# Kernel tuning notes

Measured on AMD Instinct MI355X. Metric: run time of the kernel, lower is better.

## Reference

```python
import jax, jax.numpy as jnp
import numpy as np

N, E, Z, C, B, G, T = 10000, 160000, 10, 64, 8, 16, 2
R_MAX = 5.0
AVG_NEIGH = 16.0
L_SLICES = ((0, 1), (1, 4), (4, 9))  # l=0,1,2 blocks of the 9 SH components


def sph_harm(u):
    # component-normalized real spherical harmonics up to l=2, u: [E,3] unit vectors
    x, y, z = u[:, 0], u[:, 1], u[:, 2]
    s3, s5, s15 = 3.0 ** 0.5, 5.0 ** 0.5, 15.0 ** 0.5
    return jnp.stack([
        jnp.ones_like(x),
        s3 * x, s3 * y, s3 * z,
        s15 * x * y, s15 * y * z, (s5 / 2) * (3 * z * z - 1), s15 * x * z, (s15 / 2) * (x * x - y * y),
    ], axis=1)  # [E,9]


def radial_embed(r):
    # Bessel basis * polynomial cutoff (p=5), r: [E]
    u = r / R_MAX
    n = jnp.arange(1, B + 1, dtype=jnp.float32)
    bessel = jnp.sqrt(2.0 / R_MAX) * jnp.sin(n[None, :] * jnp.pi * u[:, None]) / (r[:, None] + 1e-9)
    p = 5.0
    fc = 1 - (p + 1) * (p + 2) / 2 * u ** p + p * (p + 2) * u ** (p + 1) - p * (p + 1) / 2 * u ** (p + 2)
    fc = jnp.where(u < 1.0, fc, 0.0)
    return bessel * fc[:, None]  # [E,B]


def per_l_linear(x, W):
    # x: [n,C,9], W: [3,C,C]; independent channel mixing per l-block
    return jnp.concatenate([
        jnp.einsum('ncm,cd->ndm', x[:, :, s:e], W[l]) for l, (s, e) in enumerate(L_SLICES)
    ], axis=2)


def _forward(positions, node_attrs, charges, shifts, W_emb, atomic_energies,
             W_r1, W_r2, W_mix, W_sc, w_poly, W_prod, w_e, w_d,
             edge_index, batch, num_graphs):
    sender, receiver = edge_index[0], edge_index[1]
    # atomic reference energies
    node_e0 = node_attrs @ atomic_energies  # [N]
    e0 = jax.ops.segment_sum(node_e0, batch, num_segments=num_graphs)
    # node embedding: scalars only
    node_feats = jnp.zeros((positions.shape[0], C, 9), positions.dtype)
    node_feats = node_feats.at[:, :, 0].set(node_attrs @ W_emb)
    # edge geometry
    vec = positions[sender] - positions[receiver] + shifts  # [E,3]
    lengths = jnp.sqrt(jnp.sum(vec * vec, axis=1) + 1e-12)
    sh = sph_harm(vec / lengths[:, None])        # [E,9]
    edge_feats = radial_embed(lengths)           # [E,B]
    energies = [e0]
    dipoles = []
    for t in range(T):
        # radial MLP -> per-channel TP weights
        w = jax.nn.silu(edge_feats @ W_r1[t]) @ W_r2[t]      # [E,C]
        h_s = node_feats[sender, :, 0]                       # gather sender scalars [E,C]
        m = (w * h_s)[:, :, None] * sh[:, None, :]           # TP message [E,C,9]
        agg = jax.ops.segment_sum(m, receiver, num_segments=positions.shape[0]) / AVG_NEIGH
        msg = per_l_linear(agg, W_mix[t])
        sc = per_l_linear(node_feats, W_sc[t])               # self-connection
        # product basis (correlation 3): channel-wise scalar polynomial gate
        s0 = msg[:, :, 0]
        poly = w_poly[t, :, 0][None] + w_poly[t, :, 1][None] * s0 + w_poly[t, :, 2][None] * s0 * s0
        node_feats = per_l_linear(msg * poly[:, :, None], W_prod[t]) + sc
        # readout: 1x0e energy + 1x1o dipole
        e_n = node_feats[:, :, 0] @ w_e[t]                   # [N]
        energies.append(jax.ops.segment_sum(e_n, batch, num_segments=num_graphs))
        dipoles.append(jnp.einsum('ncm,c->nm', node_feats[:, :, 1:4], w_d[t]))  # [N,3]
    contributions = jnp.stack(energies, axis=-1)             # [G,T+1]
    total_energy = jnp.sum(contributions, axis=-1)           # [G]
    atomic_dipoles = jnp.sum(jnp.stack(dipoles, axis=-1), axis=-1)  # [N,3]
    total_dipole = jax.ops.segment_sum(atomic_dipoles, batch, num_segments=num_graphs)
    total_dipole = total_dipole + jax.ops.segment_sum(charges[:, None] * positions, batch, num_segments=num_graphs)
    return total_energy, contributions, atomic_dipoles, total_dipole


def setup_inputs():
    key = jax.random.key(0)
    ks = jax.random.split(key, 16)
    s = 0.1
    species = jax.random.randint(ks[1], (N,), 0, Z)
    return {
        'positions': jax.random.normal(ks[0], (N, 3)) * 3.0,
        'node_attrs': jax.nn.one_hot(species, Z, dtype=jnp.float32),
        'charges': jax.random.normal(ks[2], (N,)) * 0.1,
        'shifts': jnp.zeros((E, 3), jnp.float32),
        'W_emb': jax.random.normal(ks[5], (Z, C)) * s,
        'atomic_energies': jax.random.normal(ks[6], (Z,)) * s,
        'W_r1': jax.random.normal(ks[7], (T, B, 64)) * s,
        'W_r2': jax.random.normal(ks[8], (T, 64, C)) * s,
        'W_mix': jax.random.normal(ks[9], (T, 3, C, C)) * s,
        'W_sc': jax.random.normal(ks[10], (T, 3, C, C)) * s,
        'w_poly': jax.random.normal(ks[11], (T, C, 3)) * s,
        'W_prod': jax.random.normal(ks[12], (T, 3, C, C)) * s,
        'w_e': jax.random.normal(ks[13], (T, C)) * s,
        'w_d': jax.random.normal(ks[14], (T, C)) * s,
        'edge_index': jax.random.randint(ks[3], (2, E), 0, N),
        'batch': jnp.sort(jax.random.randint(ks[4], (N,), 0, G)),
        'num_graphs': G,
    }


def reference(positions, node_attrs, charges, shifts, W_emb, atomic_energies,
              W_r1, W_r2, W_mix, W_sc, w_poly, W_prod, w_e, w_d,
              edge_index, batch, num_graphs):
    args = (node_attrs, charges, shifts, W_emb, atomic_energies, W_r1, W_r2,
            W_mix, W_sc, w_poly, W_prod, w_e, w_d, edge_index, batch, num_graphs)
    total_energy, contributions, atomic_dipoles, total_dipole = _forward(positions, *args)
    forces = -jax.grad(lambda p: jnp.sum(_forward(p, *args)[0]))(positions)
    return total_energy, contributions, forces, total_dipole, atomic_dipoles
```

## Files before the change

kernel.cpp:

```cpp
#include <hip/hip_runtime.h>
#include <hip/hip_bf16.h>

#define NN 10000
#define NE 160000
#define NZ 10
#define NBES 8
#define NG 16
#define NT 2
#define NB 2048
#define NB1 2049
#define PL ((size_t)NN*64)

static constexpr float PI_F  = 3.14159265358979323846f;
static constexpr float KBES  = 0.63245553203367587f;
static constexpr float S3    = 1.73205080756887729f;

static constexpr size_t OFF_UVL  = 0;
static constexpr size_t OFF_PIN  = OFF_UVL + (size_t)NE*4;
static constexpr size_t OFF_ATT  = OFF_PIN + (size_t)NN*3;
static constexpr size_t OFF_CHG  = OFF_ATT + (size_t)NN*NZ;
static constexpr size_t OFF_SHF  = OFF_CHG + (size_t)NN;
static constexpr size_t OFF_NF0  = OFF_SHF + (size_t)NE*3;
static constexpr size_t OFF_NF1  = OFF_NF0 + PL;
static constexpr size_t OFF_MSG0 = OFF_NF1 + 4*PL;
static constexpr size_t OFF_MSG1 = OFF_MSG0 + PL;
static constexpr size_t OFF_AGG  = OFF_MSG1 + PL;
static constexpr size_t O_GA1    = OFF_AGG;
static constexpr size_t O_GA0    = OFF_AGG + 2*PL;
static constexpr size_t OFF_W    = OFF_AGG + 4*PL;
static constexpr size_t O_WEMB   = OFF_W;
static constexpr size_t O_AE     = O_WEMB + 640;
static constexpr size_t O_R1     = O_AE   + 16;
static constexpr size_t O_R2     = O_R1   + 1024;
static constexpr size_t O_WMIX   = O_R2   + 8192;
static constexpr size_t O_WMIXT  = O_WMIX + 24576;
static constexpr size_t O_WSC    = O_WMIXT+ 24576;
static constexpr size_t O_WSCT   = O_WSC  + 24576;
static constexpr size_t O_WPROD  = O_WSCT + 24576;
static constexpr size_t O_WPRODT = O_WPROD+ 24576;
static constexpr size_t O_WPOLY  = O_WPRODT+24576;
static constexpr size_t O_WE     = O_WPOLY+ 384;
static constexpr size_t O_WD     = O_WE   + 128;
static constexpr size_t OFF_ACC  = O_WD   + 128;
static constexpr size_t O_E0G    = OFF_ACC;
static constexpr size_t O_ETG    = O_E0G + 16;
static constexpr size_t O_TD     = O_ETG + 32;
static constexpr size_t O_ADP    = O_TD  + 48;
static constexpr size_t O_GPOS   = O_ADP + (size_t)NN*3;
static constexpr size_t ACC_FLOATS = 96 + (size_t)NN*6;
static constexpr size_t O_EN0    = O_GPOS + (size_t)NN*3;
static constexpr size_t O_EN1    = O_EN0 + NN;
static constexpr size_t O_E0N    = O_EN1 + NN;
static constexpr size_t O_FLAG   = O_E0N + NN;
static constexpr size_t O_TW     = O_FLAG + 4;
static constexpr size_t O_TQ     = O_TW + (size_t)2*NB1*64;
static constexpr size_t O_OFFR   = O_TQ + (size_t)2*NB1*64;
static constexpr size_t O_OFFS   = O_OFFR + (NN+1);
static constexpr size_t O_CURR   = O_OFFS + (NN+1);
static constexpr size_t O_CURS   = O_CURR + NN;
static constexpr size_t O_RECRAW = O_CURS + NN;
static constexpr size_t O_RECR   = (O_RECRAW + 7) & ~(size_t)7;
static constexpr size_t O_RECS   = O_RECR + (size_t)NE*8;
static constexpr size_t WS_FLOATS= O_RECS + (size_t)NE*8;

__device__ __forceinline__ float rlane(float v, int l){
  return __int_as_float(__builtin_amdgcn_readlane(__float_as_int(v), l));
}

static constexpr int LD_CNT[14] = {NN*3, NN*NZ, NN, NE*3, NZ*64, NZ, NT*NBES*64, NT*64*64,
                                   NT*3*64*64, NT*3*64*64, NT*64*3, NT*3*64*64, NT*64, NT*64};
static constexpr int LD_TOTAL = NN*3 + NN*NZ + NN + NE*3 + NZ*64 + NZ + NT*NBES*64 + NT*64*64
                              + 3*(NT*3*64*64) + NT*64*3 + 4*(NT*64) - NT*64*2;
__global__ __launch_bounds__(256) void k_load_all(
    const void* s0, const void* s1, const void* s2, const void* s3, const void* s4,
    const void* s5, const void* s6, const void* s7, const void* s8, const void* s9,
    const void* s10, const void* s11, const void* s12, const void* s13,
    float* __restrict__ ws){
  __shared__ int found;
  if (threadIdx.x == 0) found = 0;
  __syncthreads();
  const unsigned* raw = (const unsigned*)s1;
  int f = 0;
  for (int i = threadIdx.x; i < 4096; i += 256){
    unsigned w = raw[i];
    f |= (w == 0x00003F80u || w == 0x3F803F80u) ? 1 : 0;
  }
  if (f) found = 1;
  __syncthreads();
  const int isbf = found;
  if (blockIdx.x == 0 && threadIdx.x == 0) ((int*)(ws + O_FLAG))[0] = isbf;

  const void* srcs[14] = {s0,s1,s2,s3,s4,s5,s6,s7,s8,s9,s10,s11,s12,s13};
  const size_t dsts[14] = {OFF_PIN, OFF_ATT, OFF_CHG, OFF_SHF, O_WEMB, O_AE, O_R1, O_R2,
                           O_WMIX, O_WSC, O_WPOLY, O_WPROD, O_WE, O_WD};
  int i = blockIdx.x*256 + threadIdx.x;
  int seg = -1, off = i;
  #pragma unroll
  for (int j = 0; j < 14; ++j){
    if (seg < 0){
      if (off < LD_CNT[j]) seg = j;
      else off -= LD_CNT[j];
    }
  }
  if (seg < 0) return;
  float v = isbf ? __bfloat162float(((const __hip_bfloat16*)srcs[seg])[off])
                 : ((const float*)srcs[seg])[off];
  ws[dsts[seg] + off] = v;
}

static constexpr int GEOM_B = (NE+255)/256;
static constexpr int TAB_B  = (2*NB1+3)/4;
static constexpr int INIT_B = (NN+3)/4;
static constexpr int TRAN_B = 5*4096/256;
__global__ __launch_bounds__(256, 3) void k_prep(float* __restrict__ ws, const int* __restrict__ ei){
  int b = blockIdx.x;
  if (b < GEOM_B){
    int e = b*256 + threadIdx.x;
    if (e >= NE) return;
    const float* pos = ws + OFF_PIN;
    const float* shifts = ws + OFF_SHF;
    int s = ei[e], r = ei[NE + e];
    float vx = pos[s*3+0] - pos[r*3+0] + shifts[(size_t)e*3+0];
    float vy = pos[s*3+1] - pos[r*3+1] + shifts[(size_t)e*3+1];
    float vz = pos[s*3+2] - pos[r*3+2] + shifts[(size_t)e*3+2];
    float L = sqrtf(vx*vx + vy*vy + vz*vz + 1e-12f);
    float inv = 1.f / L;
    float4 uq; uq.x = vx*inv; uq.y = vy*inv; uq.z = vz*inv; uq.w = L;
    *(float4*)(ws + OFF_UVL + (size_t)e*4) = uq;
    if (L < 5.f){
      atomicAdd((int*)(ws + O_CURR) + r, 1);
      atomicAdd((int*)(ws + O_CURS) + s, 1);
    }
  } else if (b < GEOM_B + TAB_B){
    int lane = threadIdx.x & 63;
    int task = (b - GEOM_B)*4 + (threadIdx.x >> 6);
    if (task >= 2*NB1) return;
    int t = task / NB1, node = task % NB1;
    const float* R1 = ws + O_R1 + (size_t)t*512;
    const float* R2 = ws + O_R2 + (size_t)t*4096;
    float r1c[8];
    #pragma unroll
    for (int j = 0; j < 8; ++j) r1c[j] = R1[j*64 + lane];
    float L = fmaxf((float)node * (5.f/NB), 1e-6f);
    float ur = L*0.2f;
    float ef[8], dd[8];
    if (ur < 1.f){
      float u2=ur*ur, u4=u2*u2, u5=u4*ur;
      float fc = 1.f - 21.f*u5 + 35.f*u5*ur - 15.f*u5*u2;
      float omu = 1.f - ur;
      float dfc = -105.f*u4*omu*omu;
      float invr = 1.f/(L + 1e-9f);
      #pragma unroll
      for (int bb = 0; bb < 8; ++bb){
        float nb = (float)(bb+1);
        float arg = nb*PI_F*ur;
        float sn = __sinf(arg), cs = __cosf(arg);
        float bes = KBES*sn*invr;
        float dbes = KBES*(nb*PI_F*0.2f)*cs*invr - bes*invr;
        ef[bb] = bes*fc;
        dd[bb] = dbes*fc + bes*dfc*0.2f;
      }
    } else {
      #pragma unroll
      for (int bb = 0; bb < 8; ++bb){ ef[bb] = 0.f; dd[bb] = 0.f; }
    }
    float a = 0.f, tt = 0.f;
    #pragma unroll
    for (int bb = 0; bb < 8; ++bb){ a = fmaf(ef[bb], r1c[bb], a); tt = fmaf(r1c[bb], dd[bb], tt); }
    float sg = 1.f/(1.f + __expf(-a));
    float sl = a*sg;
    float q  = sg*fmaf(a, 1.f - sg, 1.f)*tt;
    float r2c[64];
    #pragma unroll
    for (int j = 0; j < 64; ++j) r2c[j] = R2[j*64 + lane];
    float W0=0.f, W1=0.f, Q0=0.f, Q1=0.f;
    #pragma unroll
    for (int j = 0; j < 64; j += 2){
      W0 = fmaf(rlane(sl, j  ), r2c[j  ], W0);
      W1 = fmaf(rlane(sl, j+1), r2c[j+1], W1);
      Q0 = fmaf(rlane(q,  j  ), r2c[j  ], Q0);
      Q1 = fmaf(rlane(q,  j+1), r2c[j+1], Q1);
    }
    size_t idx = ((size_t)t*NB1 + node)*64 + lane;
    ws[O_TW + idx] = (W0+W1)*(1.f/16.f);
    ws[O_TQ + idx] = (Q0+Q1)*(1.f/16.f);
  } else if (b < GEOM_B + TAB_B + INIT_B){
    int lane = threadIdx.x & 63;
    int n = (b - GEOM_B - TAB_B)*4 + (threadIdx.x >> 6);
    if (n >= NN) return;
    const float* attrs = ws + OFF_ATT;
    float acc = 0.f;
    #pragma unroll
    for (int z = 0; z < NZ; ++z) acc = fmaf(attrs[(size_t)n*NZ+z], ws[O_WEMB + z*64 + lane], acc);
    ws[OFF_NF0 + (size_t)n*64 + lane] = acc;
    if (lane == 0){
      float e = 0.f;
      #pragma unroll
      for (int z = 0; z < NZ; ++z) e = fmaf(attrs[(size_t)n*NZ+z], ws[O_AE + z], e);
      ws[O_E0N + n] = e;
    }
  } else {
    int i = (b - GEOM_B - TAB_B - INIT_B)*256 + threadIdx.x;
    int mat = i >> 12, r = (i >> 6) & 63, c = i & 63;
    const size_t src[5] = {O_WMIX, O_WMIX+12288, O_WPROD, O_WPROD+12288, O_WSC+12288};
    const size_t dst[5] = {O_WMIXT, O_WMIXT+12288, O_WPRODT, O_WPRODT+12288, O_WSCT+12288};
    ws[dst[mat] + (size_t)c*64 + r] = ws[src[mat] + (size_t)r*64 + c];
  }
}

__global__ __launch_bounds__(1024) void k_csr_scan(
    int* __restrict__ curr, int* __restrict__ curs,
    int* __restrict__ offr, int* __restrict__ offs_){
  __shared__ unsigned short cr[NN], cs[NN];
  __shared__ int pr[1024], ps[1024];
  int tid = threadIdx.x;
  for (int i = tid; i < NN; i += 1024){
    cr[i] = (unsigned short)curr[i];
    cs[i] = (unsigned short)curs[i];
  }
  __syncthreads();
  const int chunk = (NN + 1023)/1024;
  int lo = tid*chunk, hi = lo + chunk;
  if (hi > NN) hi = NN;
  if (lo > NN) lo = NN;
  int sr = 0, ss = 0;
  for (int i = lo; i < hi; ++i){ sr += cr[i]; ss += cs[i]; }
  pr[tid] = sr; ps[tid] = ss;
  __syncthreads();
  for (int o = 1; o < 1024; o <<= 1){
    int vr = (tid >= o) ? pr[tid-o] : 0;
    int vs = (tid >= o) ? ps[tid-o] : 0;
    __syncthreads();
    pr[tid] += vr; ps[tid] += vs;
    __syncthreads();
  }
  int runr = tid ? pr[tid-1] : 0;
  int runs = tid ? ps[tid-1] : 0;
  for (int i = lo; i < hi; ++i){
    int a = cr[i], c = cs[i];
    offr[i] = runr; curr[i] = runr; runr += a;
    offs_[i] = runs; curs[i] = runs; runs += c;
  }
  if (tid == 1023){ offr[NN] = runr; offs_[NN] = runs; }
}

__global__ void k_csr_fill(const int* __restrict__ ei, const float* __restrict__ uvl,
                           int* __restrict__ curr, int* __restrict__ curs,
                           float* __restrict__ recr, float* __restrict__ recs){
  int e = blockIdx.x*256 + threadIdx.x;
  if (e >= NE) return;
  float4 q = *(const float4*)(uvl + (size_t)e*4);
  if (q.w >= 5.f) return;
  int s = ei[e], r = ei[NE + e];
  int4 meta; meta.x = s; meta.y = r; meta.z = e; meta.w = 0;
  int pr = atomicAdd(&curr[r], 1);
  *(float4*)(recr + (size_t)pr*8) = q;
  *(int4*)(recr + (size_t)pr*8 + 4) = meta;
  int ps = atomicAdd(&curs[s], 1);
  *(float4*)(recs + (size_t)ps*8) = q;
  *(int4*)(recs + (size_t)ps*8 + 4) = meta;
}

__global__ __launch_bounds__(256) void k_agg(
    const float* __restrict__ TWt, const float* __restrict__ recr,
    const float* __restrict__ h, const int* __restrict__ offr,
    float* __restrict__ agg){
  int lane = threadIdx.x & 63;
  int wid = blockIdx.x*4 + (threadIdx.x >> 6);
  int nw  = gridDim.x*4;
  for (int n = wid; n < NN; n += nw){
    int lo = offr[n], hi = offr[n+1];
    float c0=0.f, x1=0.f, y1=0.f, z1=0.f;
    float d0=0.f, x2=0.f, y2=0.f, z2=0.f;
    int i = lo;
    for (; i+1 < hi; i += 2){
      const float4 qa = *(const float4*)(recr + (size_t)i*8);
      const int sa = __builtin_amdgcn_readfirstlane(((const int*)(recr + (size_t)i*8 + 4))[0]);
      const float4 qb = *(const float4*)(recr + (size_t)(i+1)*8);
      const int sb = __builtin_amdgcn_readfirstlane(((const int*)(recr + (size_t)(i+1)*8 + 4))[0]);
      float pa = qa.w*(NB/5.f); int ba = (int)pa; float fa = pa - (float)ba;
      float pb = qb.w*(NB/5.f); int bbq = (int)pb; float fb = pb - (float)bbq;
      const float* Ta = TWt + (size_t)ba*64 + lane;
      const float* Tb = TWt + (size_t)bbq*64 + lane;
      float ta0 = Ta[0], tb0 = Tb[0];
      float wa = fmaf(Ta[64]-ta0, fa, ta0);
      float wb = fmaf(Tb[64]-tb0, fb, tb0);
      float wha = wa * h[(size_t)sa*64 + lane];
      float whb = wb * h[(size_t)sb*64 + lane];
      c0 += wha; d0 += whb;
      x1 = fmaf(wha, qa.x, x1); x2 = fmaf(whb, qb.x, x2);
      y1 = fmaf(wha, qa.y, y1); y2 = fmaf(whb, qb.y, y2);
      z1 = fmaf(wha, qa.z, z1); z2 = fmaf(whb, qb.z, z2);
    }
    if (i < hi){
      const float4 q = *(const float4*)(recr + (size_t)i*8);
      const int sU = __builtin_amdgcn_readfirstlane(((const int*)(recr + (size_t)i*8 + 4))[0]);
      float pa = q.w*(NB/5.f); int ba = (int)pa; float fa = pa - (float)ba;
      const float* Ta = TWt + (size_t)ba*64 + lane;
      float ta0 = Ta[0];
      float wa = fmaf(Ta[64]-ta0, fa, ta0);
      float wha = wa * h[(size_t)sU*64 + lane];
      c0 += wha;
      x1 = fmaf(wha, q.x, x1);
      y1 = fmaf(wha, q.y, y1);
      z1 = fmaf(wha, q.z, z1);
    }
    size_t ob = (size_t)n*64 + lane;
    agg[ob]        = c0 + d0;
    agg[ob+PL]     = S3*(x1 + x2);
    agg[ob+2*PL]   = S3*(y1 + y2);
    agg[ob+3*PL]   = S3*(z1 + z2);
  }
}

static constexpr int NODE_GRID = 512;
template<int TI>
__global__ __launch_bounds__(256, 2) void k_node(float* __restrict__ ws){
  __shared__ float s0buf[2][64];
  const int lane = threadIdx.x & 63;
  const int k = threadIdx.x >> 6;
  const int l = (k==0) ? 0 : 1;
  const float* Wm = ws + O_WMIX  + TI*12288 + (size_t)l*4096;
  const float* Wp = ws + O_WPROD + TI*12288 + (size_t)l*4096;
  const float* Wsc= ws + O_WSC   + TI*12288 + (size_t)l*4096;
  const bool use_sc = (TI==1) || (k==0);
  float wcm[64], wcp[64], wcs[64];
  #pragma unroll
  for (int j = 0; j < 64; ++j) wcm[j] = Wm[j*64 + lane];
  #pragma unroll
  for (int j = 0; j < 64; ++j) wcp[j] = Wp[j*64 + lane];
  if (use_sc){
    #pragma unroll
    for (int j = 0; j < 64; ++j) wcs[j] = Wsc[j*64 + lane];
  }
  const float p0 = ws[O_WPOLY + TI*192 + lane*3];
  const float p1 = ws[O_WPOLY + TI*192 + lane*3 + 1];
  const float p2 = ws[O_WPOLY + TI*192 + lane*3 + 2];
  const float rw = (k==0) ? ws[O_WE + TI*64 + lane] : ws[O_WD + TI*64 + lane];
  const float* aggk = ws + OFF_AGG + (size_t)k*PL;
  const float* nfk  = (TI==0) ? (ws + OFF_NF0) : (ws + OFF_NF1 + (size_t)k*PL);
  float* msgp = ws + (TI==0 ? OFF_MSG0 : OFF_MSG1);
  float* nfo  = ws + OFF_NF1 + (size_t)k*PL;
  float* en   = ws + (TI==0 ? O_EN0 : O_EN1);
  float* adp  = ws + O_ADP;
  int it = 0;
  for (int n = blockIdx.x; n < NN; n += NODE_GRID, ++it){
    size_t base = (size_t)n*64 + lane;
    float a = aggk[base];
    float m0=0.f, m1=0.f, m2=0.f, m3=0.f;
    #pragma unroll
    for (int j = 0; j < 64; j += 4){
      m0 = fmaf(rlane(a, j  ), wcm[j  ], m0);
      m1 = fmaf(rlane(a, j+1), wcm[j+1], m1);
      m2 = fmaf(rlane(a, j+2), wcm[j+2], m2);
      m3 = fmaf(rlane(a, j+3), wcm[j+3], m3);
    }
    float m = (m0+m1) + (m2+m3);
    if (k == 0) s0buf[it & 1][lane] = m;
    __syncthreads();
    float s0 = s0buf[it & 1][lane];
    float xg = m * fmaf(fmaf(p2, s0, p1), s0, p0);
    float b0=0.f, b1=0.f;
    #pragma unroll
    for (int j = 0; j < 64; j += 2){
      b0 = fmaf(rlane(xg, j  ), wcp[j  ], b0);
      b1 = fmaf(rlane(xg, j+1), wcp[j+1], b1);
    }
    float out = b0 + b1;
    if (use_sc){
      float xs = nfk[base];
      float a0=0.f, a1=0.f;
      #pragma unroll
      for (int j = 0; j < 64; j += 2){
        a0 = fmaf(rlane(xs, j  ), wcs[j  ], a0);
        a1 = fmaf(rlane(xs, j+1), wcs[j+1], a1);
      }
      out += a0 + a1;
    }
    if (TI == 0) nfo[base] = out;
    if (k == 0) msgp[base] = s0;
    float red = out * rw;
    #pragma unroll
    for (int o = 32; o; o >>= 1) red += __shfl_xor(red, o, 64);
    if (lane == 0){
      if (k == 0) en[n] = red;
      else        adp[n*3 + (k-1)] += red;
    }
  }
}

__global__ __launch_bounds__(256, 3) void k_gback1(
    const float* __restrict__ WPRODT1, const float* __restrict__ we1,
    const float* __restrict__ msg1, const float* __restrict__ wp,
    const float* __restrict__ WMIXT1, float* __restrict__ out){
  int lane = threadIdx.x & 63;
  float wcol[64];
  #pragma unroll
  for (int j = 0; j < 64; ++j) wcol[j] = WMIXT1[j*64 + lane];
  float g = 0.f;
  #pragma unroll
  for (int c = 0; c < 64; ++c) g = fmaf(we1[c], WPRODT1[c*64 + lane], g);
  float p0 = wp[lane*3], p1 = wp[lane*3+1], p2 = wp[lane*3+2];
  int wid = blockIdx.x*4 + (threadIdx.x >> 6);
  int nw  = gridDim.x*4;
  for (int n = wid; n < NN; n += nw){
    float s0 = msg1[(size_t)n*64 + lane];
    float poly = fmaf(fmaf(p2, s0, p1), s0, p0);
    float dp   = fmaf(2.f*p2, s0, p1);
    float gb = g*fmaf(s0, dp, poly);
    float a0=0.f, a1=0.f, a2=0.f, a3=0.f;
    #pragma unroll
    for (int j = 0; j < 64; j += 4){
      a0 = fmaf(rlane(gb, j  ), wcol[j  ], a0);
      a1 = fmaf(rlane(gb, j+1), wcol[j+1], a1);
      a2 = fmaf(rlane(gb, j+2), wcol[j+2], a2);
      a3 = fmaf(rlane(gb, j+3), wcol[j+3], a3);
    }
    out[(size_t)n*64 + lane] = (a0+a1) + (a2+a3);
  }
}

static constexpr int GHG_GRID = 1024;
static constexpr int RED_B = (NN+255)/256;
__global__ __launch_bounds__(256) void k_ghg0(float* __restrict__ ws, const int* __restrict__ offs_,
                                              const int* __restrict__ batch){
  __shared__ float wl[2*4096];
  if (blockIdx.x >= GHG_GRID){
    int n = (blockIdx.x - GHG_GRID)*256 + threadIdx.x;
    int lane = threadIdx.x & 63;
    bool valid = (n < NN);
    int g = valid ? batch[n] : -1;
    float v0=0.f, v1=0.f, v2=0.f, tx=0.f, ty=0.f, tz=0.f;
    if (valid){
      v0 = ws[O_E0N + n]; v1 = ws[O_EN0 + n]; v2 = ws[O_EN1 + n];
      float qq = ws[OFF_CHG + n];
      tx = ws[O_ADP + n*3+0] + qq*ws[OFF_PIN + n*3+0];
      ty = ws[O_ADP + n*3+1] + qq*ws[OFF_PIN + n*3+1];
      tz = ws[O_ADP + n*3+2] + qq*ws[OFF_PIN + n*3+2];
    }
    float* e0g = ws + O_E0G; float* Etg = ws + O_ETG; float* td = ws + O_TD;
    int g0 = __shfl(g, 0, 64), g63 = __shfl(g, 63, 64);
    if (g0 == g63 && g0 >= 0){
      #pragma unroll
      for (int o = 32; o; o >>= 1){
        v0 += __shfl_xor(v0, o, 64); v1 += __shfl_xor(v1, o, 64); v2 += __shfl_xor(v2, o, 64);
        tx += __shfl_xor(tx, o, 64); ty += __shfl_xor(ty, o, 64); tz += __shfl_xor(tz, o, 64);
      }
      if (lane == 0){
        atomicAdd(&e0g[g0], v0); atomicAdd(&Etg[g0], v1); atomicAdd(&Etg[16+g0], v2);
        atomicAdd(&td[g0*3+0], tx); atomicAdd(&td[g0*3+1], ty); atomicAdd(&td[g0*3+2], tz);
      }
    } else if (valid){
      atomicAdd(&e0g[g], v0); atomicAdd(&Etg[g], v1); atomicAdd(&Etg[16+g], v2);
      atomicAdd(&td[g*3+0], tx); atomicAdd(&td[g*3+1], ty); atomicAdd(&td[g*3+2], tz);
    }
    return;
  }
  for (int i = threadIdx.x; i < 4096; i += 256){
    wl[i]        = ws[O_WPRODT + i];
    wl[4096 + i] = ws[O_WMIXT + i];
  }
  __syncthreads();
  const int lane = threadIdx.x & 63;
  int wid = blockIdx.x*4 + (threadIdx.x >> 6);
  const int nw = GHG_GRID*4;
  float gnfc = ws[O_WE + lane];
  {
    const float* WS1 = ws + O_WSCT + 12288;
    const float* we1 = ws + O_WE + 64;
    #pragma unroll
    for (int c = 0; c < 64; ++c) gnfc = fmaf(we1[c], WS1[c*64 + lane], gnfc);
  }
  const float p0 = ws[O_WPOLY + lane*3];
  const float p1 = ws[O_WPOLY + lane*3 + 1];
  const float p2 = ws[O_WPOLY + lane*3 + 2];
  const float* TW1 = ws + O_TW + (size_t)NB1*64;
  const float* recs = ws + O_RECS;
  const float* GA1 = ws + O_GA1;
  for (int n = wid; n < NN; n += nw){
    int lo = offs_[n], hi = offs_[n+1];
    float acc = 0.f, acc2 = 0.f;
    int i = lo;
    for (; i+1 < hi; i += 2){
      const float4 qa = *(const float4*)(recs + (size_t)i*8);
      const int ra = __builtin_amdgcn_readfirstlane(((const int*)(recs + (size_t)i*8 + 4))[1]);
      const float4 qb = *(const float4*)(recs + (size_t)(i+1)*8);
      const int rb = __builtin_amdgcn_readfirstlane(((const int*)(recs + (size_t)(i+1)*8 + 4))[1]);
      float pa = qa.w*(NB/5.f); int ba = (int)pa; float fa = pa - (float)ba;
      float pb = qb.w*(NB/5.f); int bbq = (int)pb; float fb = pb - (float)bbq;
      const float* Ta = TW1 + (size_t)ba*64 + lane;
      const float* Tb = TW1 + (size_t)bbq*64 + lane;
      float ta0 = Ta[0], tb0 = Tb[0];
      float wa = fmaf(Ta[64]-ta0, fa, ta0);
      float wb = fmaf(Tb[64]-tb0, fb, tb0);
      acc  = fmaf(wa, GA1[(size_t)ra*64 + lane], acc);
      acc2 = fmaf(wb, GA1[(size_t)rb*64 + lane], acc2);
    }
    if (i < hi){
      const float4 q = *(const float4*)(recs + (size_t)i*8);
      const int rU = __builtin_amdgcn_readfirstlane(((const int*)(recs + (size_t)i*8 + 4))[1]);
      float pa = q.w*(NB/5.f); int ba = (int)pa; float fa = pa - (float)ba;
      const float* Ta = TW1 + (size_t)ba*64 + lane;
      float ta0 = Ta[0];
      float wa = fmaf(Ta[64]-ta0, fa, ta0);
      acc = fmaf(wa, GA1[(size_t)rU*64 + lane], acc);
    }
    float gB = gnfc + (acc + acc2);
    float q0=0.f, q1=0.f;
    #pragma unroll
    for (int j = 0; j < 64; j += 2){
      q0 = fmaf(rlane(gB,j),   wl[j*64 + lane],     q0);
      q1 = fmaf(rlane(gB,j+1), wl[(j+1)*64 + lane], q1);
    }
    float gmp = q0 + q1;
    float s0v = ws[OFF_MSG0 + (size_t)n*64 + lane];
    float poly = fmaf(fmaf(p2, s0v, p1), s0v, p0);
    float dp   = fmaf(2.f*p2, s0v, p1);
    float gb = gmp * fmaf(s0v, dp, poly);
    float u0=0.f, u1=0.f;
    #pragma unroll
    for (int j = 0; j < 64; j += 2){
      u0 = fmaf(rlane(gb,j),   wl[4096 + j*64 + lane],     u0);
      u1 = fmaf(rlane(gb,j+1), wl[4096 + (j+1)*64 + lane], u1);
    }
    ws[O_GA0 + (size_t)n*64 + lane] = u0 + u1;
  }
}

__global__ __launch_bounds__(256) void k_bwdE2(float* __restrict__ ws, const int* __restrict__ nlive_ptr){
  const int lane = threadIdx.x & 63;
  int wid = blockIdx.x*4 + (threadIdx.x >> 6);
  const int nw = gridDim.x*4;
  const int nlive = nlive_ptr[0];
  const float* recs = ws + O_RECS;
  const float* TQ  = ws + O_TQ;
  const float* h0  = ws + OFF_NF0;
  const float* h1  = ws + OFF_NF1;
  const float* ga0 = ws + O_GA0;
  const float* ga1 = ws + O_GA1;
  float* gpos = ws + O_GPOS;
  for (int i = wid; i < nlive; i += nw){
    const float4 q = *(const float4*)(recs + (size_t)i*8);
    const int* meta = (const int*)(recs + (size_t)i*8 + 4);
    const int s = __builtin_amdgcn_readfirstlane(meta[0]);
    const int r = __builtin_amdgcn_readfirstlane(meta[1]);
    float posb = q.w*(NB/5.f);
    int bi = (int)posb;
    float fr = posb - (float)bi;
    const float* T0 = TQ + (size_t)bi*64 + lane;
    const float* T1 = T0 + (size_t)NB1*64;
    float Q0 = fmaf(T0[64]-T0[0], fr, T0[0]);
    float Q1 = fmaf(T1[64]-T1[0], fr, T1[0]);
    float rr = Q0*h0[(size_t)s*64 + lane]*ga0[(size_t)r*64 + lane]
             + Q1*h1[(size_t)s*64 + lane]*ga1[(size_t)r*64 + lane];
    #pragma unroll
    for (int o = 32; o; o >>= 1) rr += __shfl_xor(rr, o, 64);
    if (lane < 3){
      float u = (lane==0) ? q.x : ((lane==1) ? q.y : q.z);
      float v = rr*u;
      atomicAdd(&gpos[(size_t)s*3 + lane],  v);
      atomicAdd(&gpos[(size_t)r*3 + lane], -v);
    }
  }
}

__global__ void k_writeout(const float* __restrict__ e0g, const float* __restrict__ Etg,
                           const float* __restrict__ td, const float* __restrict__ adp,
                           const float* __restrict__ gpos, void* __restrict__ outv,
                           const int* __restrict__ flag){
  int i = blockIdx.x*256 + threadIdx.x;
  const int total = NG + NG*3 + NN*3 + NG*3 + NN*3;
  if (i >= total) return;
  float v;
  if (i < 16){
    v = e0g[i] + Etg[i] + Etg[16+i];
  } else if (i < 64){
    int j = i - 16; int g = j/3, t = j - g*3;
    v = (t == 0) ? e0g[g] : Etg[(t-1)*16 + g];
  } else if (i < 64 + NN*3){
    v = -gpos[i-64];
  } else if (i < 64 + NN*3 + 48){
    v = td[i - (64 + NN*3)];
  } else {
    v = adp[i - (64 + NN*3 + 48)];
  }
  if (flag[0]) ((__hip_bfloat16*)outv)[i] = __float2bfloat16(v);
  else         ((float*)outv)[i] = v;
}

extern "C" void kernel_launch(void* const* d_in, const int* in_sizes, int n_in,
                              void* d_out, int out_size, void* d_ws, size_t ws_size,
                              hipStream_t stream) {
  if (ws_size < WS_FLOATS*sizeof(float)) return;
  const int* ei    = (const int*)d_in[14];
  const int* batch = (const int*)d_in[15];
  float* ws = (float*)d_ws;

  int* offr  = (int*)(ws + O_OFFR);
  int* offs_ = (int*)(ws + O_OFFS);
  int* curr  = (int*)(ws + O_CURR);
  int* curs  = (int*)(ws + O_CURS);

  hipMemsetAsync(ws + OFF_ACC, 0, ACC_FLOATS*sizeof(float), stream);
  hipMemsetAsync(curr, 0, 2*NN*sizeof(int), stream);

  k_load_all<<<(LD_TOTAL+255)/256, 256, 0, stream>>>(
      d_in[0], d_in[1], d_in[2], d_in[3], d_in[4], d_in[5], d_in[6], d_in[7],
      d_in[8], d_in[9], d_in[10], d_in[11], d_in[12], d_in[13], ws);
  k_prep<<<GEOM_B + TAB_B + INIT_B + TRAN_B, 256, 0, stream>>>(ws, ei);
  k_csr_scan<<<1, 1024, 0, stream>>>(curr, curs, offr, offs_);
  k_csr_fill<<<(NE+255)/256, 256, 0, stream>>>(ei, ws+OFF_UVL, curr, curs,
                                               ws+O_RECR, ws+O_RECS);

  k_agg<<<1024, 256, 0, stream>>>(ws+O_TW, ws+O_RECR, ws+OFF_NF0, offr, ws+OFF_AGG);
  k_node<0><<<NODE_GRID, 256, 0, stream>>>(ws);
  k_agg<<<1024, 256, 0, stream>>>(ws+O_TW + (size_t)NB1*64, ws+O_RECR, ws+OFF_NF1, offr, ws+OFF_AGG);
  k_node<1><<<NODE_GRID, 256, 0, stream>>>(ws);

  k_gback1<<<1024, 256, 0, stream>>>(ws+O_WPRODT+12288, ws+O_WE+64,
                                     ws+OFF_MSG1, ws+O_WPOLY+192,
                                     ws+O_WMIXT+12288, ws+O_GA1);
  k_ghg0<<<GHG_GRID + RED_B, 256, 0, stream>>>(ws, offs_, batch);
  k_bwdE2<<<2048, 256, 0, stream>>>(ws, offs_ + NN);

  k_writeout<<<(60112+255)/256, 256, 0, stream>>>(ws+O_E0G, ws+O_ETG, ws+O_TD, ws+O_ADP,
                                                  ws+O_GPOS, d_out, (const int*)(ws+O_FLAG));
}
```

Baseline: 345.6 us.

## Split node channel-mixing across two waves per l-block and prefetch next node

The node-update kernel now uses 512 threads per block, with two waves sharing each of the four l-blocks. Each wave holds half of the weight columns (32 instead of 64 per matrix), and partial sums are combined through shared memory. The next node's aggregate and self-connection inputs are also prefetched into registers before the current node is computed. The aim is to cut per-thread register pressure and per-node latency so more waves hide memory latency, at the cost of a second __syncthreads per node and extra shared-memory traffic.

```diff
diff --git a/kernel.cpp b/kernel.cpp
--- a/kernel.cpp
+++ b/kernel.cpp
@@ -315,23 +315,27 @@
 
 static constexpr int NODE_GRID = 512;
 template<int TI>
-__global__ __launch_bounds__(256, 2) void k_node(float* __restrict__ ws){
-  __shared__ float s0buf[2][64];
+__global__ __launch_bounds__(512, 1) void k_node(float* __restrict__ ws){
+  __shared__ float pm[4][2][64];
+  __shared__ float po[4][2][64];
   const int lane = threadIdx.x & 63;
-  const int k = threadIdx.x >> 6;
+  const int w = threadIdx.x >> 6;
+  const int k = w >> 1;
+  const int h = w & 1;
   const int l = (k==0) ? 0 : 1;
+  const int j0 = h*32;
   const float* Wm = ws + O_WMIX  + TI*12288 + (size_t)l*4096;
   const float* Wp = ws + O_WPROD + TI*12288 + (size_t)l*4096;
   const float* Wsc= ws + O_WSC   + TI*12288 + (size_t)l*4096;
   const bool use_sc = (TI==1) || (k==0);
-  float wcm[64], wcp[64], wcs[64];
+  float wcm[32], wcp[32], wcs[32];
   #pragma unroll
-  for (int j = 0; j < 64; ++j) wcm[j] = Wm[j*64 + lane];
+  for (int j = 0; j < 32; ++j) wcm[j] = Wm[(j0+j)*64 + lane];
   #pragma unroll
-  for (int j = 0; j < 64; ++j) wcp[j] = Wp[j*64 + lane];
+  for (int j = 0; j < 32; ++j) wcp[j] = Wp[(j0+j)*64 + lane];
   if (use_sc){
     #pragma unroll
-    for (int j = 0; j < 64; ++j) wcs[j] = Wsc[j*64 + lane];
+    for (int j = 0; j < 32; ++j) wcs[j] = Wsc[(j0+j)*64 + lane];
   }
   const float p0 = ws[O_WPOLY + TI*192 + lane*3];
   const float p1 = ws[O_WPOLY + TI*192 + lane*3 + 1];
@@ -343,49 +347,62 @@
   float* nfo  = ws + OFF_NF1 + (size_t)k*PL;
   float* en   = ws + (TI==0 ? O_EN0 : O_EN1);
   float* adp  = ws + O_ADP;
-  int it = 0;
-  for (int n = blockIdx.x; n < NN; n += NODE_GRID, ++it){
-    size_t base = (size_t)n*64 + lane;
-    float a = aggk[base];
-    float m0=0.f, m1=0.f, m2=0.f, m3=0.f;
-    #pragma unroll
-    for (int j = 0; j < 64; j += 4){
-      m0 = fmaf(rlane(a, j  ), wcm[j  ], m0);
-      m1 = fmaf(rlane(a, j+1), wcm[j+1], m1);
-      m2 = fmaf(rlane(a, j+2), wcm[j+2], m2);
-      m3 = fmaf(rlane(a, j+3), wcm[j+3], m3);
-    }
-    float m = (m0+m1) + (m2+m3);
-    if (k == 0) s0buf[it & 1][lane] = m;
+
+  int n = blockIdx.x;
+  if (n >= NN) return;
+  float a  = aggk[(size_t)n*64 + lane];
+  float xs = use_sc ? nfk[(size_t)n*64 + lane] : 0.f;
+  for (; n < NN; ){
+    const int nn = n + NODE_GRID;
+    float a_nx = 0.f, xs_nx = 0.f;
+    if (nn < NN){
+      a_nx = aggk[(size_t)nn*64 + lane];
+      if (use_sc) xs_nx = nfk[(size_t)nn*64 + lane];
+    }
+    const size_t base = (size_t)n*64 + lane;
+    float m0=0.f, m1=0.f;
+    #pragma unroll
+    for (int j = 0; j < 32; j += 2){
+      m0 = fmaf(rlane(a, j0+j  ), wcm[j  ], m0);
+      m1 = fmaf(rlane(a, j0+j+1), wcm[j+1], m1);
+    }
+    pm[k][h][lane] = m0 + m1;
     __syncthreads();
-    float s0 = s0buf[it & 1][lane];
-    float xg = m * fmaf(fmaf(p2, s0, p1), s0, p0);
+    const float m  = pm[k][0][lane] + pm[k][1][lane];
+    const float s0 = pm[0][0][lane] + pm[0][1][lane];
+    const float xg = m * fmaf(fmaf(p2, s0, p1), s0, p0);
     float b0=0.f, b1=0.f;
     #pragma unroll
-    for (int j = 0; j < 64; j += 2){
-      b0 = fmaf(rlane(xg, j  ), wcp[j  ], b0);
-      b1 = fmaf(rlane(xg, j+1), wcp[j+1], b1);
-    }
-    float out = b0 + b1;
+    for (int j = 0; j < 32; j += 2){
+      b0 = fmaf(rlane(xg, j0+j  ), wcp[j  ], b0);
+      b1 = fmaf(rlane(xg, j0+j+1), wcp[j+1], b1);
+    }
+    float pout = b0 + b1;
     if (use_sc){
-      float xs = nfk[base];
-      float a0=0.f, a1=0.f;
+      float c0=0.f, c1=0.f;
       #pragma unroll
-      for (int j = 0; j < 64; j += 2){
-        a0 = fmaf(rlane(xs, j  ), wcs[j  ], a0);
-        a1 = fmaf(rlane(xs, j+1), wcs[j+1], a1);
+      for (int j = 0; j < 32; j += 2){
+        c0 = fmaf(rlane(xs, j0+j  ), wcs[j  ], c0);
+        c1 = fmaf(rlane(xs, j0+j+1), wcs[j+1], c1);
       }
-      out += a0 + a1;
-    }
-    if (TI == 0) nfo[base] = out;
-    if (k == 0) msgp[base] = s0;
-    float red = out * rw;
-    #pragma unroll
-    for (int o = 32; o; o >>= 1) red += __shfl_xor(red, o, 64);
-    if (lane == 0){
-      if (k == 0) en[n] = red;
-      else        adp[n*3 + (k-1)] += red;
-    }
+      pout += c0 + c1;
+    }
+    po[k][h][lane] = pout;
+    __syncthreads();
+    if (h == 0){
+      const float out = po[k][0][lane] + po[k][1][lane];
+      if (TI == 0) nfo[base] = out;
+      if (k == 0) msgp[base] = s0;
+      float red = out * rw;
+      #pragma unroll
+      for (int o = 32; o; o >>= 1) red += __shfl_xor(red, o, 64);
+      if (lane == 0){
+        if (k == 0) en[n] = red;
+        else        adp[n*3 + (k-1)] += red;
+      }
+    }
+    n = nn;
+    a = a_nx; xs = xs_nx;
   }
 }
 
@@ -613,9 +630,9 @@
                                                ws+O_RECR, ws+O_RECS);
 
   k_agg<<<1024, 256, 0, stream>>>(ws+O_TW, ws+O_RECR, ws+OFF_NF0, offr, ws+OFF_AGG);
-  k_node<0><<<NODE_GRID, 256, 0, stream>>>(ws);
+  k_node<0><<<NODE_GRID, 512, 0, stream>>>(ws);
   k_agg<<<1024, 256, 0, stream>>>(ws+O_TW + (size_t)NB1*64, ws+O_RECR, ws+OFF_NF1, offr, ws+OFF_AGG);
-  k_node<1><<<NODE_GRID, 256, 0, stream>>>(ws);
+  k_node<1><<<NODE_GRID, 512, 0, stream>>>(ws);
 
   k_gback1<<<1024, 256, 0, stream>>>(ws+O_WPRODT+12288, ws+O_WE+64,
                                      ws+OFF_MSG1, ws+O_WPOLY+192,
```

Result: slower. 390.0 us (+12.8%).
